# Kernel optimization log

Hardware: AMD Instinct MI355X
Metric: run time of the kernel (lower is better)

## Reference

```python
import jax, jax.numpy as jnp
import numpy as np

WINDOW = 5  # len_sort_window in the original module


def setup_inputs() -> dict:
    key = jax.random.key(0)
    k1, k2, k3 = jax.random.split(key, 3)
    B, L, D = 8, 4000, 512  # L divisible by WINDOW, D < L
    q = jax.random.normal(k1, (B, L, D), dtype=jnp.float32)
    k = jax.random.normal(k2, (B, L, D), dtype=jnp.float32)
    v = jax.random.normal(k3, (B, L, D), dtype=jnp.float32)
    return {"q": q, "k": k, "v": v}


def reference(q, k, v):
    # q, k are unused by the original forward.
    B, L, D = v.shape
    t = jnp.arange(L)          # sequence positions
    s = jnp.arange(D)          # per-feature cyclic shift amount (= feature index)
    # Shift feature i left by i: shifted[:, t, i] = v[:, (t + i) % L, i]
    idx_fwd = (t[:, None] + s[None, :]) % L            # [L, D]
    v_shift = jnp.take_along_axis(v, idx_fwd[None, :, :], axis=1)  # [B, L, D]
    # Sort within fixed non-overlapping windows of size WINDOW along the seq axis.
    v_sorted = jnp.sort(v_shift.reshape(B, L // WINDOW, WINDOW, D), axis=2)
    v_sorted = v_sorted.reshape(B, L, D)
    # Unshift feature i right by i: out[:, t, i] = v_sorted[:, (t - i) % L, i]
    idx_bwd = (t[:, None] - s[None, :]) % L            # [L, D]
    return jnp.take_along_axis(v_sorted, idx_bwd[None, :, :], axis=1)
```

## Files before the change

### kernel.cpp

```cpp
#include <hip/hip_runtime.h>


constexpr int L  = 4000;
constexpr int D  = 512;
constexpr int SROWS   = 50;
constexpr int NG      = SROWS / 5;
constexpr int NSTRIPS = L / SROWS;

#define CE(a, b) { float lo_ = fminf(a, b); float hi_ = fmaxf(a, b); (a) = lo_; (b) = hi_; }

__global__ __launch_bounds__(256, 6)
void swd18_ring(const float* __restrict__ v, float* __restrict__ out) {
    const int nwg = gridDim.x * gridDim.y;
    const int lid = blockIdx.x + gridDim.x * blockIdx.y;
    const int q   = nwg >> 3;
    const int rm  = nwg & 7;
    const int xcd = lid & 7;
    const int pos = lid >> 3;
    const int nid = (xcd < rm ? xcd * (q + 1) : rm * (q + 1) + (xcd - rm) * q) + pos;

    const int b     = nid / (NSTRIPS * 2);
    const int rr    = nid % (NSTRIPS * 2);
    const int half  = rr & 1;
    const int strip = rr >> 1;
    const int i     = half * 256 + threadIdx.x;

    const float* __restrict__ vb = v   + (size_t)b * (L * D);
    float*       __restrict__ ob = out + (size_t)b * (L * D);

    const int R0 = strip * SROWS;

    float s[5][5];

    auto loadg = [&](int slot, int g) {
        int row = R0 + 5 * g;
        if (row < 0)  row += L;
        if (row >= L) row -= L;
#pragma unroll
        for (int j = 0; j < 5; ++j)
            s[slot][j] = vb[(size_t)(row + j) * D + i];
    };

    loadg(0, -1);
    loadg(1,  0);
    loadg(2,  1);
    loadg(3,  2);

    const int rc = i % 5;
    const bool e0 = rc == 0, e1 = rc == 1, e2 = rc == 2, e3 = rc == 3;

#pragma unroll
    for (int k = 0; k < NG; ++k) {
        if (k + 3 <= NG)
            loadg((k + 4) % 5, k + 3);

        const float* P = s[k % 5];
        const float* C = s[(k + 1) % 5];
        const float* N = s[(k + 2) % 5];

        float A0 = e0 ? P[0] : e1 ? P[1] : e2 ? P[2] : e3 ? P[3] : P[4];
        float A1 = e0 ? P[1] : e1 ? P[2] : e2 ? P[3] : e3 ? P[4] : C[0];
        float A2 = e0 ? P[2] : e1 ? P[3] : e2 ? P[4] : e3 ? C[0] : C[1];
        float A3 = e0 ? P[3] : e1 ? P[4] : e2 ? C[0] : e3 ? C[1] : C[2];
        float A4 = e0 ? P[4] : e1 ? C[0] : e2 ? C[1] : e3 ? C[2] : C[3];
        float B0 = e0 ? C[0] : e1 ? C[1] : e2 ? C[2] : e3 ? C[3] : C[4];
        float B1 = e0 ? C[1] : e1 ? C[2] : e2 ? C[3] : e3 ? C[4] : N[0];
        float B2 = e0 ? C[2] : e1 ? C[3] : e2 ? C[4] : e3 ? N[0] : N[1];
        float B3 = e0 ? C[3] : e1 ? C[4] : e2 ? N[0] : e3 ? N[1] : N[2];
        float B4 = e0 ? C[4] : e1 ? N[0] : e2 ? N[1] : e3 ? N[2] : N[3];

        CE(A0, A1) CE(A3, A4) CE(A2, A4) CE(A2, A3) CE(A1, A4)
        CE(A0, A3) CE(A0, A2) CE(A1, A3) CE(A1, A2)
        CE(B0, B1) CE(B3, B4) CE(B2, B4) CE(B2, B3) CE(B1, B4)
        CE(B0, B3) CE(B0, B2) CE(B1, B3) CE(B1, B2)

        float f0 = e0 ? B0 : e1 ? A4 : e2 ? A3 : e3 ? A2 : A1;
        float f1 = e0 ? B1 : e1 ? B0 : e2 ? A4 : e3 ? A3 : A2;
        float f2 = e0 ? B2 : e1 ? B1 : e2 ? B0 : e3 ? A4 : A3;
        float f3 = e0 ? B3 : e1 ? B2 : e2 ? B1 : e3 ? B0 : A4;
        float f4 = e0 ? B4 : e1 ? B3 : e2 ? B2 : e3 ? B1 : B0;

        float* o = ob + (size_t)(R0 + 5 * k) * D + i;
        __builtin_nontemporal_store(f0, o + 0 * D);
        __builtin_nontemporal_store(f1, o + 1 * D);
        __builtin_nontemporal_store(f2, o + 2 * D);
        __builtin_nontemporal_store(f3, o + 3 * D);
        __builtin_nontemporal_store(f4, o + 4 * D);
    }
}

#undef CE

extern "C" void kernel_launch(void* const* d_in, const int* in_sizes, int n_in,
                              void* d_out, int out_size, void* d_ws, size_t ws_size,
                              hipStream_t stream) {
    const float* v = (const float*)d_in[2];
    float* out = (float*)d_out;

    const int B = in_sizes[2] / (L * D);
    dim3 grid(NSTRIPS * 2, B);
    swd18_ring<<<grid, dim3(256), 0, stream>>>(v, out);
}
```

Measured before the change: 181.4 us.

## Vectorize to float4 columns with one 5-row output window per thread

```diff
diff --git a/kernel.cpp b/kernel.cpp
--- a/kernel.cpp
+++ b/kernel.cpp
@@ -1,92 +1,84 @@
 #include <hip/hip_runtime.h>
 
 
-constexpr int L  = 4000;
-constexpr int D  = 512;
-constexpr int SROWS   = 50;
-constexpr int NG      = SROWS / 5;
-constexpr int NSTRIPS = L / SROWS;
+constexpr int L   = 4000;
+constexpr int D   = 512;
+constexpr int NW  = L / 5;
+constexpr int WPB = 2;
+constexpr int NBX = NW / WPB;
+
+typedef float f4 __attribute__((ext_vector_type(4)));
 
 #define CE(a, b) { float lo_ = fminf(a, b); float hi_ = fmaxf(a, b); (a) = lo_; (b) = hi_; }
 
-__global__ __launch_bounds__(256, 6)
-void swd18_ring(const float* __restrict__ v, float* __restrict__ out) {
+__global__ __launch_bounds__(256, 4)
+void swd18_f4(const float* __restrict__ v, float* __restrict__ out) {
     const int nwg = gridDim.x * gridDim.y;
     const int lid = blockIdx.x + gridDim.x * blockIdx.y;
-    const int q   = nwg >> 3;
-    const int rm  = nwg & 7;
+    const int qq  = nwg >> 3;
     const int xcd = lid & 7;
     const int pos = lid >> 3;
-    const int nid = (xcd < rm ? xcd * (q + 1) : rm * (q + 1) + (xcd - rm) * q) + pos;
+    const int nid = xcd * qq + pos;
 
-    const int b     = nid / (NSTRIPS * 2);
-    const int rr    = nid % (NSTRIPS * 2);
-    const int half  = rr & 1;
-    const int strip = rr >> 1;
-    const int i     = half * 256 + threadIdx.x;
+    const int b  = nid / NBX;
+    const int bx = nid % NBX;
 
-    const float* __restrict__ vb = v   + (size_t)b * (L * D);
-    float*       __restrict__ ob = out + (size_t)b * (L * D);
+    const int w  = WPB * bx + (threadIdx.x >> 7);
+    const int q  = threadIdx.x & 127;
+    const int c0 = q << 2;
+    const int R0 = 5 * w;
 
-    const int R0 = strip * SROWS;
+    const f4* __restrict__ vb4 = (const f4*)(v   + (size_t)b * (L * D));
+    f4*       __restrict__ ob4 = (f4*)      (out + (size_t)b * (L * D));
 
-    float s[5][5];
-
-    auto loadg = [&](int slot, int g) {
-        int row = R0 + 5 * g;
+    f4 in[14];
+#pragma unroll
+    for (int r = 0; r < 14; ++r) {
+        int row = R0 - 5 + r;
         if (row < 0)  row += L;
         if (row >= L) row -= L;
-#pragma unroll
-        for (int j = 0; j < 5; ++j)
-            s[slot][j] = vb[(size_t)(row + j) * D + i];
-    };
+        in[r] = vb4[(size_t)row * (D / 4) + q];
+    }
 
-    loadg(0, -1);
-    loadg(1,  0);
-    loadg(2,  1);
-    loadg(3,  2);
+    const int rc0 = c0 % 5;
+    f4 o0, o1, o2, o3, o4;
 
-    const int rc = i % 5;
-    const bool e0 = rc == 0, e1 = rc == 1, e2 = rc == 2, e3 = rc == 3;
+#define COMP(J, F) do {                                                         \
+    int rcj = rc0 + (J); if (rcj >= 5) rcj -= 5;                                \
+    const bool e0 = rcj == 0, e1 = rcj == 1, e2 = rcj == 2, e3 = rcj == 3;      \
+    float A0 = e0 ? in[0].F : e1 ? in[1].F : e2 ? in[2].F : e3 ? in[3].F : in[4].F;   \
+    float A1 = e0 ? in[1].F : e1 ? in[2].F : e2 ? in[3].F : e3 ? in[4].F : in[5].F;   \
+    float A2 = e0 ? in[2].F : e1 ? in[3].F : e2 ? in[4].F : e3 ? in[5].F : in[6].F;   \
+    float A3 = e0 ? in[3].F : e1 ? in[4].F : e2 ? in[5].F : e3 ? in[6].F : in[7].F;   \
+    float A4 = e0 ? in[4].F : e1 ? in[5].F : e2 ? in[6].F : e3 ? in[7].F : in[8].F;   \
+    float B0 = e0 ? in[5].F : e1 ? in[6].F : e2 ? in[7].F : e3 ? in[8].F : in[9].F;   \
+    float B1 = e0 ? in[6].F : e1 ? in[7].F : e2 ? in[8].F : e3 ? in[9].F : in[10].F;  \
+    float B2 = e0 ? in[7].F : e1 ? in[8].F : e2 ? in[9].F : e3 ? in[10].F : in[11].F; \
+    float B3 = e0 ? in[8].F : e1 ? in[9].F : e2 ? in[10].F : e3 ? in[11].F : in[12].F;\
+    float B4 = e0 ? in[9].F : e1 ? in[10].F : e2 ? in[11].F : e3 ? in[12].F : in[13].F;\
+    CE(A0, A1) CE(A3, A4) CE(A2, A4) CE(A2, A3) CE(A1, A4)                      \
+    CE(A0, A3) CE(A0, A2) CE(A1, A3) CE(A1, A2)                                 \
+    CE(B0, B1) CE(B3, B4) CE(B2, B4) CE(B2, B3) CE(B1, B4)                      \
+    CE(B0, B3) CE(B0, B2) CE(B1, B3) CE(B1, B2)                                 \
+    o0.F = e0 ? B0 : e1 ? A4 : e2 ? A3 : e3 ? A2 : A1;                          \
+    o1.F = e0 ? B1 : e1 ? B0 : e2 ? A4 : e3 ? A3 : A2;                          \
+    o2.F = e0 ? B2 : e1 ? B1 : e2 ? B0 : e3 ? A4 : A3;                          \
+    o3.F = e0 ? B3 : e1 ? B2 : e2 ? B1 : e3 ? B0 : A4;                          \
+    o4.F = e0 ? B4 : e1 ? B3 : e2 ? B2 : e3 ? B1 : B0;                          \
+} while (0)
 
-#pragma unroll
-    for (int k = 0; k < NG; ++k) {
-        if (k + 3 <= NG)
-            loadg((k + 4) % 5, k + 3);
+    COMP(0, x);
+    COMP(1, y);
+    COMP(2, z);
+    COMP(3, w);
+#undef COMP
 
-        const float* P = s[k % 5];
-        const float* C = s[(k + 1) % 5];
-        const float* N = s[(k + 2) % 5];
-
-        float A0 = e0 ? P[0] : e1 ? P[1] : e2 ? P[2] : e3 ? P[3] : P[4];
-        float A1 = e0 ? P[1] : e1 ? P[2] : e2 ? P[3] : e3 ? P[4] : C[0];
-        float A2 = e0 ? P[2] : e1 ? P[3] : e2 ? P[4] : e3 ? C[0] : C[1];
-        float A3 = e0 ? P[3] : e1 ? P[4] : e2 ? C[0] : e3 ? C[1] : C[2];
-        float A4 = e0 ? P[4] : e1 ? C[0] : e2 ? C[1] : e3 ? C[2] : C[3];
-        float B0 = e0 ? C[0] : e1 ? C[1] : e2 ? C[2] : e3 ? C[3] : C[4];
-        float B1 = e0 ? C[1] : e1 ? C[2] : e2 ? C[3] : e3 ? C[4] : N[0];
-        float B2 = e0 ? C[2] : e1 ? C[3] : e2 ? C[4] : e3 ? N[0] : N[1];
-        float B3 = e0 ? C[3] : e1 ? C[4] : e2 ? N[0] : e3 ? N[1] : N[2];
-        float B4 = e0 ? C[4] : e1 ? N[0] : e2 ? N[1] : e3 ? N[2] : N[3];
-
-        CE(A0, A1) CE(A3, A4) CE(A2, A4) CE(A2, A3) CE(A1, A4)
-        CE(A0, A3) CE(A0, A2) CE(A1, A3) CE(A1, A2)
-        CE(B0, B1) CE(B3, B4) CE(B2, B4) CE(B2, B3) CE(B1, B4)
-        CE(B0, B3) CE(B0, B2) CE(B1, B3) CE(B1, B2)
-
-        float f0 = e0 ? B0 : e1 ? A4 : e2 ? A3 : e3 ? A2 : A1;
-        float f1 = e0 ? B1 : e1 ? B0 : e2 ? A4 : e3 ? A3 : A2;
-        float f2 = e0 ? B2 : e1 ? B1 : e2 ? B0 : e3 ? A4 : A3;
-        float f3 = e0 ? B3 : e1 ? B2 : e2 ? B1 : e3 ? B0 : A4;
-        float f4 = e0 ? B4 : e1 ? B3 : e2 ? B2 : e3 ? B1 : B0;
-
-        float* o = ob + (size_t)(R0 + 5 * k) * D + i;
-        __builtin_nontemporal_store(f0, o + 0 * D);
-        __builtin_nontemporal_store(f1, o + 1 * D);
-        __builtin_nontemporal_store(f2, o + 2 * D);
-        __builtin_nontemporal_store(f3, o + 3 * D);
-        __builtin_nontemporal_store(f4, o + 4 * D);
-    }
+    f4* o = ob4 + (size_t)R0 * (D / 4) + q;
+    __builtin_nontemporal_store(o0, o + 0 * (D / 4));
+    __builtin_nontemporal_store(o1, o + 1 * (D / 4));
+    __builtin_nontemporal_store(o2, o + 2 * (D / 4));
+    __builtin_nontemporal_store(o3, o + 3 * (D / 4));
+    __builtin_nontemporal_store(o4, o + 4 * (D / 4));
 }
 
 #undef CE
@@ -98,6 +90,6 @@
     float* out = (float*)d_out;
 
     const int B = in_sizes[2] / (L * D);
-    dim3 grid(NSTRIPS * 2, B);
-    swd18_ring<<<grid, dim3(256), 0, stream>>>(v, out);
+    dim3 grid(NBX, B);
+    swd18_f4<<<grid, dim3(256), 0, stream>>>(v, out);
 }
```

Result: no change. 184.8 us (+1.9%).
